# Optimization experiments

Hardware: AMD Instinct MI355X
Metric: run time of the kernel (lower is better)

## Reference

```python
import jax, jax.numpy as jnp
import numpy as np
from jax import lax

EPS = 1e-5
B = 512

def _conv(x, w, pad):
    # x: [B,Cin,H,W], w: [Cout,Cin,kh,kw]
    return lax.conv_general_dilated(x, w, (1, 1), [(pad, pad), (pad, pad)],
                                    dimension_numbers=('NCHW', 'OIHW', 'NCHW'))

def _bn2d(x, g, b, m, v):
    s = g * lax.rsqrt(v + EPS)
    return x * s[None, :, None, None] + (b - m * s)[None, :, None, None]

def _bn1d(x, g, b, m, v):
    s = g * lax.rsqrt(v + EPS)
    return x * s + (b - m * s)

def _pool2(x):
    return lax.reduce_window(x, -jnp.inf, lax.max, (1, 1, 2, 2), (1, 1, 2, 2), 'VALID')

def setup_inputs() -> dict:
    key = jax.random.key(0)
    ks = iter(jax.random.split(key, 64))
    rn = lambda shape, s=1.0: jax.random.normal(next(ks), shape, dtype=jnp.float32) * s
    un = lambda shape: jax.random.uniform(next(ks), shape, dtype=jnp.float32, minval=0.5, maxval=1.5)
    def bn_params(c):
        return (jnp.ones((c,), jnp.float32), jnp.zeros((c,), jnp.float32), rn((c,), 0.1), un((c,)))
    inp = {"x": rn((B, 3, 64, 64))}
    inp["w1"] = rn((32, 3, 5, 5), 0.1)
    inp["bn1_g"], inp["bn1_b"], inp["bn1_m"], inp["bn1_v"] = bn_params(32)
    inp["w2"] = rn((64, 32, 3, 3), 0.06)
    inp["bn2_g"], inp["bn2_b"], inp["bn2_m"], inp["bn2_v"] = bn_params(64)
    inp["w3"] = rn((128, 64, 3, 3), 0.04)
    inp["bn3_g"], inp["bn3_b"], inp["bn3_m"], inp["bn3_v"] = bn_params(128)
    inp["fc_w"] = rn((256, 8192), 0.01)
    inp["fc_b"] = jnp.zeros((256,), jnp.float32)
    inp["bnf_g"], inp["bnf_b"], inp["bnf_m"], inp["bnf_v"] = bn_params(256)
    inp["c_w1"] = rn((64, 256), 0.06)
    inp["c_b1"] = jnp.zeros((64,), jnp.float32)
    inp["bnc_g"], inp["bnc_b"], inp["bnc_m"], inp["bnc_v"] = bn_params(64)
    inp["c_w2"] = rn((1, 64), 0.1)
    inp["c_b2"] = jnp.zeros((1,), jnp.float32)
    inp["m_w1"] = rn((64, 256), 0.06)
    inp["m_b1"] = jnp.zeros((64,), jnp.float32)
    inp["bnm_g"], inp["bnm_b"], inp["bnm_m"], inp["bnm_v"] = bn_params(64)
    inp["m_w2"] = rn((1, 64), 0.1)
    inp["m_b2"] = jnp.zeros((1,), jnp.float32)
    return inp

def reference(x, w1, bn1_g, bn1_b, bn1_m, bn1_v,
              w2, bn2_g, bn2_b, bn2_m, bn2_v,
              w3, bn3_g, bn3_b, bn3_m, bn3_v,
              fc_w, fc_b, bnf_g, bnf_b, bnf_m, bnf_v,
              c_w1, c_b1, bnc_g, bnc_b, bnc_m, bnc_v, c_w2, c_b2,
              m_w1, m_b1, bnm_g, bnm_b, bnm_m, bnm_v, m_w2, m_b2):
    # Block 1: conv5x5(3->32) + BN + ReLU + maxpool2 -> [B,32,32,32]
    h = _pool2(jax.nn.relu(_bn2d(_conv(x, w1, 2), bn1_g, bn1_b, bn1_m, bn1_v)))
    # Block 2: conv3x3(32->64) + BN + ReLU + maxpool2 -> [B,64,16,16]
    h = _pool2(jax.nn.relu(_bn2d(_conv(h, w2, 1), bn2_g, bn2_b, bn2_m, bn2_v)))
    # Block 3: conv3x3(64->128) + BN + ReLU + maxpool2 + ToDense -> [B,128,8,8]
    h = _pool2(jax.nn.relu(_bn2d(_conv(h, w3, 1), bn3_g, bn3_b, bn3_m, bn3_v)))
    f = h.reshape(h.shape[0], -1)  # [B, 8192]
    s = jax.nn.relu(_bn1d(f @ fc_w.T + fc_b, bnf_g, bnf_b, bnf_m, bnf_v))  # [B,256]
    c = jax.nn.relu(_bn1d(s @ c_w1.T + c_b1, bnc_g, bnc_b, bnc_m, bnc_v)) @ c_w2.T + c_b2
    mo = jax.nn.relu(_bn1d(s @ m_w1.T + m_b1, bnm_g, bnm_b, bnm_m, bnm_v)) @ m_w2.T + m_b2
    return (c, mo)  # ([B,1], [B,1])
```

## Files before the change

kernel.cpp:

```cpp
#include <hip/hip_runtime.h>
#include <hip/hip_bf16.h>

#define EPS 1e-5f

typedef __attribute__((ext_vector_type(8))) short bf16x8;
typedef __attribute__((ext_vector_type(4))) float f32x4;

__device__ __forceinline__ ushort f2b(float f) {
    return __builtin_bit_cast(ushort, __float2bfloat16(f));
}
__device__ __forceinline__ bf16x8 ld_frag(const void* p) {
    return __builtin_bit_cast(bf16x8, *reinterpret_cast<const uint4*>(p));
}

__global__ __launch_bounds__(256) void k_prep_all(
    const float* __restrict__ w1, const float* __restrict__ w2,
    const float* __restrict__ w3, const float* __restrict__ fcw,
    const float* __restrict__ x,
    const float* __restrict__ bn1g, const float* __restrict__ bn1b,
    const float* __restrict__ bn1m, const float* __restrict__ bn1v,
    const float* __restrict__ bn2g, const float* __restrict__ bn2b,
    const float* __restrict__ bn2m, const float* __restrict__ bn2v,
    const float* __restrict__ bn3g, const float* __restrict__ bn3b,
    const float* __restrict__ bn3m, const float* __restrict__ bn3v,
    ushort* __restrict__ w1p, ushort* __restrict__ w2p, ushort* __restrict__ w3p,
    float* __restrict__ b1f, float* __restrict__ b2f, float* __restrict__ b3f,
    ushort* __restrict__ fcwp, ushort* __restrict__ x4p,
    ushort* __restrict__ h1p, ushort* __restrict__ h2p)
{
    __shared__ ushort l[128 * 66];
    const int bid = blockIdx.x, t = threadIdx.x;
    if (bid < 128) {
        if (bid == 0 && t < 224) {
            if (t < 32) {
                const float s = bn1g[t] * rsqrtf(bn1v[t] + EPS);
                b1f[t] = bn1b[t] - bn1m[t] * s;
            } else if (t < 96) {
                const int c = t - 32;
                const float s = bn2g[c] * rsqrtf(bn2v[c] + EPS);
                b2f[c] = bn2b[c] - bn2m[c] * s;
            } else {
                const int c = t - 96;
                const float s = bn3g[c] * rsqrtf(bn3v[c] + EPS);
                b3f[c] = bn3b[c] - bn3m[c] * s;
            }
        }
        const int total = 5120 + 18432 + 73728;
        for (int i = bid * 256 + t; i < total; i += 128 * 256) {
            if (i < 5120) {
                const int ky = i >> 10, co = (i >> 5) & 31, k = i & 31;
                const int kx = k >> 2, ci = k & 3;
                float v = 0.f;
                if (kx < 5 && ci < 3) v = w1[((co * 3 + ci) * 5 + ky) * 5 + kx];
                const float s = bn1g[co] * rsqrtf(bn1v[co] + EPS);
                w1p[i] = f2b(v * s);
            } else if (i < 5120 + 18432) {
                const int j = i - 5120;
                const int tap = j >> 11, co = (j >> 5) & 63, ci = j & 31;
                const float s = bn2g[co] * rsqrtf(bn2v[co] + EPS);
                w2p[j] = f2b(w2[(co * 32 + ci) * 9 + tap] * s);
            } else {
                const int j = i - (5120 + 18432);
                const int tap = j >> 13, co = (j >> 6) & 127, ci = j & 63;
                const float s = bn3g[co] * rsqrtf(bn3v[co] + EPS);
                w3p[j] = f2b(w3[(co * 64 + ci) * 9 + tap] * s);
            }
        }
    } else if (bid < 384) {
        const int j = bid - 128;
        const float* src = fcw + (size_t)j * 8192;
        #pragma unroll
        for (int i = 0; i < 32; ++i) {
            const int idx = i * 256 + t;
            const int c = idx >> 6, p = idx & 63;
            l[c * 66 + p] = f2b(src[idx]);
        }
        __syncthreads();
        ushort* dst = fcwp + (size_t)j * 8192;
        #pragma unroll
        for (int i = 0; i < 32; ++i) {
            const int idx = i * 256 + t;
            const int c = idx & 127, p = idx >> 7;
            dst[idx] = l[c * 66 + p];
        }
    } else if (bid < 4480) {
        for (int p = (bid - 384) * 256 + t; p < 2506752; p += 4096 * 256) {
            const int n = p / 4896;
            const int rem = p - n * 4896;
            const int row = rem / 72, col = rem - row * 72;
            const int gr = row - 2, gc = col - 2;
            ushort4 pk; pk.x = 0; pk.y = 0; pk.z = 0; pk.w = 0;
            if ((unsigned)gr < 64u && (unsigned)gc < 64u) {
                const size_t base = ((size_t)n * 3 << 12) + (gr << 6) + gc;
                pk.x = f2b(x[base]); pk.y = f2b(x[base + 4096]); pk.z = f2b(x[base + 8192]);
            }
            *reinterpret_cast<ushort4*>(&x4p[(size_t)p * 4]) = pk;
        }
    } else if (bid < 4736) {
        const uint4 z = {0, 0, 0, 0};
        for (int i = (bid - 4480) * 256 + t; i < 270336; i += 256 * 256) {
            const int img = i / 528;
            const int rem = i - img * 528;
            const int px = rem >> 2, gg = rem & 3;
            int row, col;
            if (px < 34)      { row = 0;  col = px; }
            else if (px < 68) { row = 33; col = px - 34; }
            else { const int q = px - 68; row = 1 + (q >> 1); col = (q & 1) ? 33 : 0; }
            *reinterpret_cast<uint4*>(&h1p[(((size_t)img * 34 + row) * 34 + col) * 32 + gg * 8]) = z;
        }
    } else if (bid < 4992) {
        const uint4 z = {0, 0, 0, 0};
        for (int i = (bid - 4736) * 256 + t; i < 278528; i += 256 * 256) {
            const int img = i / 544;
            const int rem = i - img * 544;
            const int px = rem >> 3, gg = rem & 7;
            int row, col;
            if (px < 18)      { row = 0;  col = px; }
            else if (px < 36) { row = 17; col = px - 18; }
            else { const int q = px - 36; row = 1 + (q >> 1); col = (q & 1) ? 17 : 0; }
            *reinterpret_cast<uint4*>(&h2p[(((size_t)img * 18 + row) * 18 + col) * 64 + gg * 8]) = z;
        }
    }
}

__global__ __launch_bounds__(256, 4) void k_conv1(
    const ushort* __restrict__ x4p, const ushort* __restrict__ w1p,
    const float* __restrict__ bias, ushort* __restrict__ h1p)
{
    __shared__ __align__(16) ushort xs[12 * 72 * 4];
    const int bid = blockIdx.x;
    const int n = bid >> 3, q = bid & 7;
    const int t = threadIdx.x;
    const int wave = t >> 6, lane = t & 63;
    const int g = lane >> 4, l15 = lane & 15;

    {
        const ushort* src = x4p + ((size_t)(n * 68 + 8 * q) * 72) * 4;
        for (int i = t; i < 432; i += 256)
            *reinterpret_cast<uint4*>(&xs[i * 8]) = *reinterpret_cast<const uint4*>(src + i * 8);
    }
    __syncthreads();

    f32x4 acc[8][2];
    #pragma unroll
    for (int i = 0; i < 8; ++i) { acc[i][0] = (f32x4){0,0,0,0}; acc[i][1] = (f32x4){0,0,0,0}; }

    const char* xsb = (const char*)xs;
    #pragma unroll
    for (int ky = 0; ky < 5; ++ky) {
        bf16x8 a[8], b[2];
        #pragma unroll
        for (int mt = 0; mt < 8; ++mt) {
            const int crl = 2 * wave + (mt >> 2);
            const int ccl = (mt & 3) * 16 + l15;
            const int off = ((crl + ky) * 72 + ccl) * 8 + g * 16;
            const uint2 lo = *reinterpret_cast<const uint2*>(xsb + off);
            const uint2 hi = *reinterpret_cast<const uint2*>(xsb + off + 8);
            uint4 all; all.x = lo.x; all.y = lo.y; all.z = hi.x; all.w = hi.y;
            a[mt] = __builtin_bit_cast(bf16x8, all);
        }
        #pragma unroll
        for (int nt = 0; nt < 2; ++nt) {
            const int co = nt * 16 + l15;
            b[nt] = ld_frag(&w1p[(ky * 32 + co) * 32 + g * 8]);
        }
        #pragma unroll
        for (int mt = 0; mt < 8; ++mt)
            #pragma unroll
            for (int nt = 0; nt < 2; ++nt)
                acc[mt][nt] = __builtin_amdgcn_mfma_f32_16x16x32_bf16(a[mt], b[nt], acc[mt][nt], 0, 0, 0);
    }

    const int prow = q * 4 + wave;
    #pragma unroll
    for (int nt = 0; nt < 2; ++nt) {
        const int co = nt * 16 + l15;
        const float bsv = bias[co];
        #pragma unroll
        for (int mt = 0; mt < 4; ++mt) {
            #pragma unroll
            for (int j = 0; j < 2; ++j) {
                const float v0 = fmaxf(acc[mt][nt][2 * j]     + bsv, 0.f);
                const float v1 = fmaxf(acc[mt][nt][2 * j + 1] + bsv, 0.f);
                const float v2 = fmaxf(acc[mt + 4][nt][2 * j]     + bsv, 0.f);
                const float v3 = fmaxf(acc[mt + 4][nt][2 * j + 1] + bsv, 0.f);
                const int ppc = mt * 8 + g * 2 + j;
                h1p[(((size_t)n * 34 + prow + 1) * 34 + ppc + 1) * 32 + co] =
                    f2b(fmaxf(fmaxf(v0, v1), fmaxf(v2, v3)));
            }
        }
    }
}

__global__ __launch_bounds__(256, 4) void k_conv2(
    const ushort* __restrict__ h1p, const ushort* __restrict__ w2p,
    const float* __restrict__ bias, ushort* __restrict__ h2p)
{
    __shared__ __align__(16) ushort xs[10 * 34 * 32];
    const int bid = blockIdx.x;
    const int n = bid >> 2, q = bid & 3;
    const int t = threadIdx.x;
    const int wave = t >> 6, lane = t & 63;
    const int g = lane >> 4, l15 = lane & 15;
    const char* xsb = (const char*)xs;

    {
        const ushort* src = h1p + ((size_t)(n * 34 + 8 * q) * 34) * 32;
        for (int i = t; i < 1360; i += 256) {
            const int gg = i & 3, pix = i >> 2;
            const uint4 v = *reinterpret_cast<const uint4*>(src + i * 8);
            *reinterpret_cast<uint4*>((char*)xs + pix * 64 + ((gg ^ ((pix >> 1) & 3)) << 4)) = v;
        }
    }
    __syncthreads();

    f32x4 acc[4][4];
    #pragma unroll
    for (int i = 0; i < 4; ++i)
        #pragma unroll
        for (int j = 0; j < 4; ++j) acc[i][j] = (f32x4){0,0,0,0};

    #pragma unroll
    for (int tap = 0; tap < 9; ++tap) {
        const int ky = tap / 3, kx = tap - 3 * ky;
        bf16x8 a[4], b[4];
        #pragma unroll
        for (int mt = 0; mt < 4; ++mt) {
            const int crl = 2 * wave + (mt >> 1);
            const int ccl = (mt & 1) * 16 + l15;
            const int pix = (crl + ky) * 34 + ccl + kx;
            a[mt] = ld_frag(xsb + pix * 64 + ((g ^ ((pix >> 1) & 3)) << 4));
        }
        #pragma unroll
        for (int nt = 0; nt < 4; ++nt) {
            const int co = nt * 16 + l15;
            b[nt] = ld_frag(&w2p[(tap * 64 + co) * 32 + g * 8]);
        }
        #pragma unroll
        for (int mt = 0; mt < 4; ++mt)
            #pragma unroll
            for (int nt = 0; nt < 4; ++nt)
                acc[mt][nt] = __builtin_amdgcn_mfma_f32_16x16x32_bf16(a[mt], b[nt], acc[mt][nt], 0, 0, 0);
    }

    const int prow = q * 4 + wave;
    #pragma unroll
    for (int nt = 0; nt < 4; ++nt) {
        const int co = nt * 16 + l15;
        const float bsv = bias[co];
        #pragma unroll
        for (int mtl = 0; mtl < 2; ++mtl) {
            #pragma unroll
            for (int j = 0; j < 2; ++j) {
                const float v0 = fmaxf(acc[mtl][nt][2 * j]     + bsv, 0.f);
                const float v1 = fmaxf(acc[mtl][nt][2 * j + 1] + bsv, 0.f);
                const float v2 = fmaxf(acc[mtl + 2][nt][2 * j]     + bsv, 0.f);
                const float v3 = fmaxf(acc[mtl + 2][nt][2 * j + 1] + bsv, 0.f);
                const int ppc = mtl * 8 + g * 2 + j;
                h2p[(((size_t)n * 18 + prow + 1) * 18 + ppc + 1) * 64 + co] =
                    f2b(fmaxf(fmaxf(v0, v1), fmaxf(v2, v3)));
            }
        }
    }
}

__global__ __launch_bounds__(256, 4) void k_conv3(
    const ushort* __restrict__ h2p, const ushort* __restrict__ w3p,
    const float* __restrict__ bias, ushort* __restrict__ h3)
{
    __shared__ __align__(16) ushort xs[324 * 32];
    const int bid = blockIdx.x;
    const int n = bid >> 1, ch = bid & 1;
    const int t = threadIdx.x;
    const int wave = t >> 6, lane = t & 63;
    const int g = lane >> 4, l15 = lane & 15;
    const char* xsb = (const char*)xs;

    f32x4 acc[4][4];
    #pragma unroll
    for (int i = 0; i < 4; ++i)
        #pragma unroll
        for (int j = 0; j < 4; ++j) acc[i][j] = (f32x4){0,0,0,0};

    for (int gci = 0; gci < 2; ++gci) {
        if (gci) __syncthreads();
        for (int i = t; i < 1296; i += 256) {
            const int gg = i & 3, pix = i >> 2;
            const uint4 v = *reinterpret_cast<const uint4*>(
                &h2p[((size_t)n * 324 + pix) * 64 + gci * 32 + gg * 8]);
            *reinterpret_cast<uint4*>((char*)xs + pix * 64 + ((gg ^ ((pix >> 1) & 3)) << 4)) = v;
        }
        __syncthreads();
        #pragma unroll
        for (int tap = 0; tap < 9; ++tap) {
            const int ky = tap / 3, kx = tap - 3 * ky;
            bf16x8 a[4], b[4];
            #pragma unroll
            for (int mt = 0; mt < 4; ++mt) {
                const int pr = 4 * wave + mt;
                const int pix = (pr + ky) * 18 + l15 + kx;
                a[mt] = ld_frag(xsb + pix * 64 + ((g ^ ((pix >> 1) & 3)) << 4));
            }
            #pragma unroll
            for (int nt = 0; nt < 4; ++nt) {
                const int co = ch * 64 + nt * 16 + l15;
                b[nt] = ld_frag(&w3p[((size_t)(tap * 128 + co)) * 64 + gci * 32 + g * 8]);
            }
            #pragma unroll
            for (int mt = 0; mt < 4; ++mt)
                #pragma unroll
                for (int nt = 0; nt < 4; ++nt)
                    acc[mt][nt] = __builtin_amdgcn_mfma_f32_16x16x32_bf16(a[mt], b[nt], acc[mt][nt], 0, 0, 0);
        }
    }

    #pragma unroll
    for (int nt = 0; nt < 4; ++nt) {
        const int co = ch * 64 + nt * 16 + l15;
        const float bsv = bias[co];
        #pragma unroll
        for (int mtl = 0; mtl < 2; ++mtl) {
            #pragma unroll
            for (int j = 0; j < 2; ++j) {
                const int mt = mtl * 2;
                const float v0 = fmaxf(acc[mt][nt][2 * j]     + bsv, 0.f);
                const float v1 = fmaxf(acc[mt][nt][2 * j + 1] + bsv, 0.f);
                const float v2 = fmaxf(acc[mt + 1][nt][2 * j]     + bsv, 0.f);
                const float v3 = fmaxf(acc[mt + 1][nt][2 * j + 1] + bsv, 0.f);
                const int ppr = 2 * wave + mtl;
                const int pcol = g * 2 + j;
                h3[(((size_t)n * 8 + ppr) * 8 + pcol) * 128 + co] =
                    f2b(fmaxf(fmaxf(v0, v1), fmaxf(v2, v3)));
            }
        }
    }
}

__global__ __launch_bounds__(256) void k_fc(
    const ushort* __restrict__ A, const ushort* __restrict__ Bw, float* __restrict__ C)
{
    __shared__ __align__(16) ushort As[64 * 32];
    __shared__ __align__(16) ushort Bs[64 * 32];
    const int bm = blockIdx.x, bn = blockIdx.y, kz = blockIdx.z;
    const int t = threadIdx.x;
    const int wave = t >> 6, lane = t & 63;
    const int g = lane >> 4, l15 = lane & 15;

    f32x4 acc[4];
    #pragma unroll
    for (int i = 0; i < 4; ++i) acc[i] = (f32x4){0,0,0,0};

    const char* asb = (const char*)As;
    const char* bsb = (const char*)Bs;
    for (int kk = 0; kk < 16; ++kk) {
        const int k0 = kz * 512 + kk * 32;
        if (kk) __syncthreads();
        {
            const int gg = t & 3, row = t >> 2;
            const uint4 va = *reinterpret_cast<const uint4*>(
                &A[(size_t)(bm * 64 + row) * 8192 + k0 + gg * 8]);
            *reinterpret_cast<uint4*>((char*)As + row * 64 + ((gg ^ ((row >> 1) & 3)) << 4)) = va;
            const uint4 vb = *reinterpret_cast<const uint4*>(
                &Bw[(size_t)(bn * 64 + row) * 8192 + k0 + gg * 8]);
            *reinterpret_cast<uint4*>((char*)Bs + row * 64 + ((gg ^ ((row >> 1) & 3)) << 4)) = vb;
        }
        __syncthreads();
        bf16x8 a[4], b;
        #pragma unroll
        for (int mt = 0; mt < 4; ++mt) {
            const int r = mt * 16 + l15;
            a[mt] = ld_frag(asb + r * 64 + ((g ^ ((r >> 1) & 3)) << 4));
        }
        {
            const int r = wave * 16 + l15;
            b = ld_frag(bsb + r * 64 + ((g ^ ((r >> 1) & 3)) << 4));
        }
        #pragma unroll
        for (int mt = 0; mt < 4; ++mt)
            acc[mt] = __builtin_amdgcn_mfma_f32_16x16x32_bf16(a[mt], b, acc[mt], 0, 0, 0);
    }

    float* Cp = C + (size_t)kz * 512 * 256;
    const int col = bn * 64 + wave * 16 + l15;
    #pragma unroll
    for (int mt = 0; mt < 4; ++mt) {
        #pragma unroll
        for (int r = 0; r < 4; ++r) {
            const int row = bm * 64 + mt * 16 + g * 4 + r;
            Cp[(size_t)row * 256 + col] = acc[mt][r];
        }
    }
}

__global__ __launch_bounds__(128) void k_heads(
    const float* __restrict__ sraw, const float* __restrict__ fcb,
    const float* __restrict__ fg, const float* __restrict__ fb,
    const float* __restrict__ fm, const float* __restrict__ fv,
    const float* __restrict__ cw1, const float* __restrict__ cb1,
    const float* __restrict__ cg, const float* __restrict__ cbb,
    const float* __restrict__ cm, const float* __restrict__ cv,
    const float* __restrict__ cw2, const float* __restrict__ cb2,
    const float* __restrict__ mw1, const float* __restrict__ mb1,
    const float* __restrict__ mg, const float* __restrict__ mbb,
    const float* __restrict__ mm, const float* __restrict__ mv,
    const float* __restrict__ mw2, const float* __restrict__ mb2,
    float* __restrict__ outp)
{
    __shared__ float sv[256];
    const int b = blockIdx.x, t = threadIdx.x;
    for (int k = t; k < 256; k += 128) {
        float val = fcb[k];
        #pragma unroll
        for (int z = 0; z < 16; ++z) val += sraw[(size_t)z * 131072 + b * 256 + k];
        const float s = fg[k] * rsqrtf(fv[k] + EPS);
        sv[k] = fmaxf(fmaf(val, s, fb[k] - fm[k] * s), 0.f);
    }
    __syncthreads();
    const int j = t & 63;
    const bool isM = (t >= 64);
    const float* w1  = isM ? mw1 : cw1;
    const float* b1  = isM ? mb1 : cb1;
    const float* g1  = isM ? mg  : cg;
    const float* bb1 = isM ? mbb : cbb;
    const float* m1  = isM ? mm  : cm;
    const float* v1  = isM ? mv  : cv;
    const float* w2  = isM ? mw2 : cw2;
    const float* b2  = isM ? mb2 : cb2;
    float d = 0.f;
    const float* wr = w1 + j * 256;
    #pragma unroll 8
    for (int k = 0; k < 256; ++k) d = fmaf(sv[k], wr[k], d);
    d += b1[j];
    const float s1 = g1[j] * rsqrtf(v1[j] + EPS);
    d = fmaxf(fmaf(d, s1, bb1[j] - m1[j] * s1), 0.f);
    float prod = d * w2[j];
    #pragma unroll
    for (int off = 32; off > 0; off >>= 1) prod += __shfl_down(prod, off);
    if (j == 0) outp[(isM ? 512 : 0) + b] = prod + b2[0];
}

extern "C" void kernel_launch(void* const* d_in, const int* in_sizes, int n_in,
                              void* d_out, int out_size, void* d_ws, size_t ws_size,
                              hipStream_t stream)
{
    const float* x    = (const float*)d_in[0];
    const float* w1   = (const float*)d_in[1];
    const float* bn1g = (const float*)d_in[2];
    const float* bn1b = (const float*)d_in[3];
    const float* bn1m = (const float*)d_in[4];
    const float* bn1v = (const float*)d_in[5];
    const float* w2   = (const float*)d_in[6];
    const float* bn2g = (const float*)d_in[7];
    const float* bn2b = (const float*)d_in[8];
    const float* bn2m = (const float*)d_in[9];
    const float* bn2v = (const float*)d_in[10];
    const float* w3   = (const float*)d_in[11];
    const float* bn3g = (const float*)d_in[12];
    const float* bn3b = (const float*)d_in[13];
    const float* bn3m = (const float*)d_in[14];
    const float* bn3v = (const float*)d_in[15];
    const float* fcw  = (const float*)d_in[16];
    const float* fcb  = (const float*)d_in[17];
    const float* bnfg = (const float*)d_in[18];
    const float* bnfb = (const float*)d_in[19];
    const float* bnfm = (const float*)d_in[20];
    const float* bnfv = (const float*)d_in[21];
    const float* cw1  = (const float*)d_in[22];
    const float* cb1  = (const float*)d_in[23];
    const float* bncg = (const float*)d_in[24];
    const float* bncb = (const float*)d_in[25];
    const float* bncm = (const float*)d_in[26];
    const float* bncv = (const float*)d_in[27];
    const float* cw2  = (const float*)d_in[28];
    const float* cb2  = (const float*)d_in[29];
    const float* mw1  = (const float*)d_in[30];
    const float* mb1  = (const float*)d_in[31];
    const float* bnmg = (const float*)d_in[32];
    const float* bnmb = (const float*)d_in[33];
    const float* bnmm = (const float*)d_in[34];
    const float* bnmv = (const float*)d_in[35];
    const float* mw2  = (const float*)d_in[36];
    const float* mb2  = (const float*)d_in[37];

    char* W = (char*)d_ws;
    ushort* x4p  = (ushort*)(W);
    ushort* h1p  = (ushort*)(W + 20054016);
    ushort* h2p  = (ushort*)(W + 57933824);
    ushort* h3   = (ushort*)(W + 79167488);
    ushort* w1p  = (ushort*)(W + 87556096);
    ushort* w2p  = (ushort*)(W + 87566336);
    ushort* w3p  = (ushort*)(W + 87603200);
    ushort* fcwp = (ushort*)(W + 87750656);
    float*  b1f  = (float*) (W + 91944960);
    float*  b2f  = (float*) (W + 91945088);
    float*  b3f  = (float*) (W + 91945344);
    float*  sr   = (float*) (W + 91946496);
    float* outp = (float*)d_out;

    k_prep_all<<<4992, 256, 0, stream>>>(w1, w2, w3, fcw, x,
                                         bn1g, bn1b, bn1m, bn1v,
                                         bn2g, bn2b, bn2m, bn2v,
                                         bn3g, bn3b, bn3m, bn3v,
                                         w1p, w2p, w3p, b1f, b2f, b3f,
                                         fcwp, x4p, h1p, h2p);
    k_conv1<<<512 * 8, 256, 0, stream>>>(x4p, w1p, b1f, h1p);
    k_conv2<<<512 * 4, 256, 0, stream>>>(h1p, w2p, b2f, h2p);
    k_conv3<<<512 * 2, 256, 0, stream>>>(h2p, w3p, b3f, h3);
    k_fc<<<dim3(8, 4, 16), 256, 0, stream>>>(h3, fcwp, sr);
    k_heads<<<512, 128, 0, stream>>>(sr, fcb, bnfg, bnfb, bnfm, bnfv,
                                     cw1, cb1, bncg, bncb, bncm, bncv, cw2, cb2,
                                     mw1, mb1, bnmg, bnmb, bnmm, bnmv, mw2, mb2, outp);
}
```

Measured before the change: 285.0 us.

## Stage conv weights in swizzled LDS per kernel row instead of global loads

The three conv kernels now stage weight fragments in shared memory, using an XOR swizzle on 16-byte chunks, instead of each wave reading B fragments directly from global memory. conv2 and conv3 load one kernel row (three taps) at a time, which adds extra __syncthreads barriers per row. The aim is to cut repeated global/L2 weight traffic across waves and get conflict-free LDS reads. The launch_bounds occupancy hint of 4 is dropped, and both that and the added LDS use can lower how many blocks run per CU.

```diff
diff --git a/kernel.cpp b/kernel.cpp
--- a/kernel.cpp
+++ b/kernel.cpp
@@ -123,11 +123,12 @@
     }
 }
 
-__global__ __launch_bounds__(256, 4) void k_conv1(
+__global__ __launch_bounds__(256) void k_conv1(
     const ushort* __restrict__ x4p, const ushort* __restrict__ w1p,
     const float* __restrict__ bias, ushort* __restrict__ h1p)
 {
     __shared__ __align__(16) ushort xs[12 * 72 * 4];
+    __shared__ __align__(16) ushort ws[5 * 32 * 32];
     const int bid = blockIdx.x;
     const int n = bid >> 3, q = bid & 7;
     const int t = threadIdx.x;
@@ -139,6 +140,12 @@
         for (int i = t; i < 432; i += 256)
             *reinterpret_cast<uint4*>(&xs[i * 8]) = *reinterpret_cast<const uint4*>(src + i * 8);
     }
+    for (int i = t; i < 640; i += 256) {
+        const int gg = i & 3, r = i >> 2;
+        const int co = r & 31;
+        const uint4 v = *reinterpret_cast<const uint4*>(&w1p[r * 32 + gg * 8]);
+        *reinterpret_cast<uint4*>((char*)ws + r * 64 + ((gg ^ ((co >> 1) & 3)) << 4)) = v;
+    }
     __syncthreads();
 
     f32x4 acc[8][2];
@@ -146,6 +153,7 @@
     for (int i = 0; i < 8; ++i) { acc[i][0] = (f32x4){0,0,0,0}; acc[i][1] = (f32x4){0,0,0,0}; }
 
     const char* xsb = (const char*)xs;
+    const char* wsb = (const char*)ws;
     #pragma unroll
     for (int ky = 0; ky < 5; ++ky) {
         bf16x8 a[8], b[2];
@@ -162,7 +170,7 @@
         #pragma unroll
         for (int nt = 0; nt < 2; ++nt) {
             const int co = nt * 16 + l15;
-            b[nt] = ld_frag(&w1p[(ky * 32 + co) * 32 + g * 8]);
+            b[nt] = ld_frag(wsb + (ky * 32 + co) * 64 + ((g ^ ((co >> 1) & 3)) << 4));
         }
         #pragma unroll
         for (int mt = 0; mt < 8; ++mt)
@@ -192,17 +200,19 @@
     }
 }
 
-__global__ __launch_bounds__(256, 4) void k_conv2(
+__global__ __launch_bounds__(256) void k_conv2(
     const ushort* __restrict__ h1p, const ushort* __restrict__ w2p,
     const float* __restrict__ bias, ushort* __restrict__ h2p)
 {
     __shared__ __align__(16) ushort xs[10 * 34 * 32];
+    __shared__ __align__(16) ushort ws[3 * 64 * 32];
     const int bid = blockIdx.x;
     const int n = bid >> 2, q = bid & 3;
     const int t = threadIdx.x;
     const int wave = t >> 6, lane = t & 63;
     const int g = lane >> 4, l15 = lane & 15;
     const char* xsb = (const char*)xs;
+    const char* wsb = (const char*)ws;
 
     {
         const ushort* src = h1p + ((size_t)(n * 34 + 8 * q) * 34) * 32;
@@ -212,7 +222,6 @@
             *reinterpret_cast<uint4*>((char*)xs + pix * 64 + ((gg ^ ((pix >> 1) & 3)) << 4)) = v;
         }
     }
-    __syncthreads();
 
     f32x4 acc[4][4];
     #pragma unroll
@@ -220,27 +229,36 @@
         #pragma unroll
         for (int j = 0; j < 4; ++j) acc[i][j] = (f32x4){0,0,0,0};
 
-    #pragma unroll
-    for (int tap = 0; tap < 9; ++tap) {
-        const int ky = tap / 3, kx = tap - 3 * ky;
-        bf16x8 a[4], b[4];
-        #pragma unroll
-        for (int mt = 0; mt < 4; ++mt) {
-            const int crl = 2 * wave + (mt >> 1);
-            const int ccl = (mt & 1) * 16 + l15;
-            const int pix = (crl + ky) * 34 + ccl + kx;
-            a[mt] = ld_frag(xsb + pix * 64 + ((g ^ ((pix >> 1) & 3)) << 4));
-        }
-        #pragma unroll
-        for (int nt = 0; nt < 4; ++nt) {
-            const int co = nt * 16 + l15;
-            b[nt] = ld_frag(&w2p[(tap * 64 + co) * 32 + g * 8]);
-        }
-        #pragma unroll
-        for (int mt = 0; mt < 4; ++mt)
-            #pragma unroll
-            for (int nt = 0; nt < 4; ++nt)
-                acc[mt][nt] = __builtin_amdgcn_mfma_f32_16x16x32_bf16(a[mt], b[nt], acc[mt][nt], 0, 0, 0);
+    for (int ky = 0; ky < 3; ++ky) {
+        if (ky) __syncthreads();
+        for (int i = t; i < 768; i += 256) {
+            const int gg = i & 3, rl = i >> 2;
+            const int co = rl & 63;
+            const uint4 v = *reinterpret_cast<const uint4*>(&w2p[(ky * 192 + rl) * 32 + gg * 8]);
+            *reinterpret_cast<uint4*>((char*)ws + rl * 64 + ((gg ^ ((co >> 1) & 3)) << 4)) = v;
+        }
+        __syncthreads();
+        #pragma unroll
+        for (int kx = 0; kx < 3; ++kx) {
+            bf16x8 a[4], b[4];
+            #pragma unroll
+            for (int mt = 0; mt < 4; ++mt) {
+                const int crl = 2 * wave + (mt >> 1);
+                const int ccl = (mt & 1) * 16 + l15;
+                const int pix = (crl + ky) * 34 + ccl + kx;
+                a[mt] = ld_frag(xsb + pix * 64 + ((g ^ ((pix >> 1) & 3)) << 4));
+            }
+            #pragma unroll
+            for (int nt = 0; nt < 4; ++nt) {
+                const int co = nt * 16 + l15;
+                b[nt] = ld_frag(wsb + (kx * 64 + co) * 64 + ((g ^ ((co >> 1) & 3)) << 4));
+            }
+            #pragma unroll
+            for (int mt = 0; mt < 4; ++mt)
+                #pragma unroll
+                for (int nt = 0; nt < 4; ++nt)
+                    acc[mt][nt] = __builtin_amdgcn_mfma_f32_16x16x32_bf16(a[mt], b[nt], acc[mt][nt], 0, 0, 0);
+        }
     }
 
     const int prow = q * 4 + wave;
@@ -264,17 +282,19 @@
     }
 }
 
-__global__ __launch_bounds__(256, 4) void k_conv3(
+__global__ __launch_bounds__(256) void k_conv3(
     const ushort* __restrict__ h2p, const ushort* __restrict__ w3p,
     const float* __restrict__ bias, ushort* __restrict__ h3)
 {
     __shared__ __align__(16) ushort xs[324 * 32];
+    __shared__ __align__(16) ushort ws[3 * 64 * 32];
     const int bid = blockIdx.x;
     const int n = bid >> 1, ch = bid & 1;
     const int t = threadIdx.x;
     const int wave = t >> 6, lane = t & 63;
     const int g = lane >> 4, l15 = lane & 15;
     const char* xsb = (const char*)xs;
+    const char* wsb = (const char*)ws;
 
     f32x4 acc[4][4];
     #pragma unroll
@@ -283,34 +303,44 @@
         for (int j = 0; j < 4; ++j) acc[i][j] = (f32x4){0,0,0,0};
 
     for (int gci = 0; gci < 2; ++gci) {
-        if (gci) __syncthreads();
-        for (int i = t; i < 1296; i += 256) {
-            const int gg = i & 3, pix = i >> 2;
-            const uint4 v = *reinterpret_cast<const uint4*>(
-                &h2p[((size_t)n * 324 + pix) * 64 + gci * 32 + gg * 8]);
-            *reinterpret_cast<uint4*>((char*)xs + pix * 64 + ((gg ^ ((pix >> 1) & 3)) << 4)) = v;
-        }
-        __syncthreads();
-        #pragma unroll
-        for (int tap = 0; tap < 9; ++tap) {
-            const int ky = tap / 3, kx = tap - 3 * ky;
-            bf16x8 a[4], b[4];
-            #pragma unroll
-            for (int mt = 0; mt < 4; ++mt) {
-                const int pr = 4 * wave + mt;
-                const int pix = (pr + ky) * 18 + l15 + kx;
-                a[mt] = ld_frag(xsb + pix * 64 + ((g ^ ((pix >> 1) & 3)) << 4));
-            }
-            #pragma unroll
-            for (int nt = 0; nt < 4; ++nt) {
-                const int co = ch * 64 + nt * 16 + l15;
-                b[nt] = ld_frag(&w3p[((size_t)(tap * 128 + co)) * 64 + gci * 32 + g * 8]);
-            }
-            #pragma unroll
-            for (int mt = 0; mt < 4; ++mt)
+        for (int ky = 0; ky < 3; ++ky) {
+            if (gci || ky) __syncthreads();
+            if (ky == 0) {
+                for (int i = t; i < 1296; i += 256) {
+                    const int gg = i & 3, pix = i >> 2;
+                    const uint4 v = *reinterpret_cast<const uint4*>(
+                        &h2p[((size_t)n * 324 + pix) * 64 + gci * 32 + gg * 8]);
+                    *reinterpret_cast<uint4*>((char*)xs + pix * 64 + ((gg ^ ((pix >> 1) & 3)) << 4)) = v;
+                }
+            }
+            for (int i = t; i < 768; i += 256) {
+                const int gg = i & 3, rl = i >> 2;
+                const int tapl = rl >> 6, co = rl & 63;
+                const uint4 v = *reinterpret_cast<const uint4*>(
+                    &w3p[((size_t)((ky * 3 + tapl) * 128 + ch * 64 + co) << 6) + gci * 32 + gg * 8]);
+                *reinterpret_cast<uint4*>((char*)ws + rl * 64 + ((gg ^ ((co >> 1) & 3)) << 4)) = v;
+            }
+            __syncthreads();
+            #pragma unroll
+            for (int kx = 0; kx < 3; ++kx) {
+                bf16x8 a[4], b[4];
                 #pragma unroll
-                for (int nt = 0; nt < 4; ++nt)
-                    acc[mt][nt] = __builtin_amdgcn_mfma_f32_16x16x32_bf16(a[mt], b[nt], acc[mt][nt], 0, 0, 0);
+                for (int mt = 0; mt < 4; ++mt) {
+                    const int pr = 4 * wave + mt;
+                    const int pix = (pr + ky) * 18 + l15 + kx;
+                    a[mt] = ld_frag(xsb + pix * 64 + ((g ^ ((pix >> 1) & 3)) << 4));
+                }
+                #pragma unroll
+                for (int nt = 0; nt < 4; ++nt) {
+                    const int co = nt * 16 + l15;
+                    b[nt] = ld_frag(wsb + (kx * 64 + co) * 64 + ((g ^ ((co >> 1) & 3)) << 4));
+                }
+                #pragma unroll
+                for (int mt = 0; mt < 4; ++mt)
+                    #pragma unroll
+                    for (int nt = 0; nt < 4; ++nt)
+                        acc[mt][nt] = __builtin_amdgcn_mfma_f32_16x16x32_bf16(a[mt], b[nt], acc[mt][nt], 0, 0, 0);
+            }
         }
     }
 
```

After: 245.5 us. 1.16x faster.
